# Kernel optimization log

Hardware: AMD Instinct MI355X
Metric: run time of the kernel (lower is better)

Reference implementation:

```python
import jax, jax.numpy as jnp
import numpy as np

EPS = 1e-06


def setup_inputs() -> dict:
    key = jax.random.key(0)
    k1, k2, k3 = jax.random.split(key, 3)
    B, V = 2048, 128
    pred_severity = jax.random.normal(k1, (B, V), dtype=jnp.float32)
    target_severity = jax.random.normal(k2, (B, V), dtype=jnp.float32)
    visit_mask = jax.random.randint(k3, (B, V), 0, 2).astype(jnp.int32)
    return {
        "pred_severity": pred_severity,
        "target_severity": target_severity,
        "visit_mask": visit_mask,
    }


def reference(pred_severity, target_severity, visit_mask):
    # pred_severity, target_severity: [B, V]; visit_mask: [B, V] (0/1)
    p, t = pred_severity, target_severity
    valid = visit_mask.astype(bool)
    V = p.shape[1]

    # Entry (b, i, j): delta_t = t[j] - t[i], dp = p[i] - p[j]
    dt = t[:, None, :] - t[:, :, None]          # [B, V, V]
    dp = p[:, :, None] - p[:, None, :]          # [B, V, V]
    sign = jnp.sign(dt)
    loss = jax.nn.softplus(-dp * sign)          # [B, V, V]

    tri = jnp.triu(jnp.ones((V, V), dtype=bool), k=1)  # ordered pairs i < j
    mask = (valid[:, :, None] & valid[:, None, :]
            & (jnp.abs(dt) > EPS) & tri)        # [B, V, V]

    total = jnp.sum(jnp.where(mask, loss, jnp.zeros((), loss.dtype)))
    count = jnp.sum(mask).astype(loss.dtype)
    return jnp.where(count > 0, total / count, jnp.zeros((), loss.dtype))
```

## Files before the change

kernel.cpp:

```cpp
#include <hip/hip_runtime.h>
#include <math.h>

#define PRL_EPS   1e-6f
#define PRL_B     2048
#define PRL_V     128
#define PRL_LOG2E 1.44269504088896340736f
#define PRL_LN2   0.69314718055994530942f

__global__ __launch_bounds__(256) void prl_pairs_kernel(
    const float* __restrict__ pred,
    const float* __restrict__ targ,
    const int*   __restrict__ mask,
    float*        __restrict__ psum,
    unsigned int* __restrict__ pcnt)
{
    __shared__ float2 rowdup[2][256];

    const int tid = threadIdx.x;
    const int r   = tid >> 7;
    const int x   = tid & 127;
    const int b   = blockIdx.x * 2 + r;

    const size_t base = (size_t)b * PRL_V + x;
    const float p  = pred[base];
    const float t  = targ[base];
    const int   m  = mask[base];
    const float tm = m ? t : __int_as_float(0x7fc00000);

    const float2 own = make_float2(p, tm);
    rowdup[r][x]       = own;
    rowdup[r][x + 128] = own;
    __syncthreads();

    const float2* __restrict__ rp = &rowdup[r][x];

    float        s[3] = {0.0f, 0.0f, 0.0f};
    unsigned int c[3] = {0u, 0u, 0u};

    for (int d0 = 1; d0 < 64; d0 += 9) {
        #pragma unroll
        for (int u = 0; u < 9; ++u) {
            const float2 e = rp[d0 + u];
            const float dt = e.y - tm;
            const float dp = p - e.x;
            const bool valid = fabsf(dt) > PRL_EPS;
            const float xx = (dt > 0.0f) ? -dp : dp;
            const float y  = xx * PRL_LOG2E;
            const float lg = __log2f(1.0f + exp2f(y));
            s[u % 3] += valid ? lg : 0.0f;
            c[u % 3] += valid ? 1u : 0u;
        }
    }
    if (x < 64) {
        const float2 e = rp[64];
        const float dt = e.y - tm;
        const float dp = p - e.x;
        const bool valid = fabsf(dt) > PRL_EPS;
        const float xx = (dt > 0.0f) ? -dp : dp;
        const float y  = xx * PRL_LOG2E;
        const float lg = __log2f(1.0f + exp2f(y));
        s[0] += valid ? lg : 0.0f;
        c[0] += valid ? 1u : 0u;
    }

    float        sum = (s[0] + s[1]) + s[2];
    unsigned int cnt = (c[0] + c[1]) + c[2];

    #pragma unroll
    for (int o = 32; o > 0; o >>= 1) {
        sum += __shfl_down(sum, o);
        cnt += __shfl_down(cnt, o);
    }

    __shared__ float        wsum[4];
    __shared__ unsigned int wcnt[4];
    const int wid  = tid >> 6;
    const int lane = tid & 63;
    if (lane == 0) { wsum[wid] = sum; wcnt[wid] = cnt; }
    __syncthreads();

    if (tid == 0) {
        psum[blockIdx.x] = (wsum[0] + wsum[1] + wsum[2] + wsum[3]) * PRL_LN2;
        pcnt[blockIdx.x] = wcnt[0] + wcnt[1] + wcnt[2] + wcnt[3];
    }
}

__global__ __launch_bounds__(256) void prl_reduce_kernel(
    const float*        __restrict__ psum,
    const unsigned int* __restrict__ pcnt,
    float* __restrict__ out)
{
    const int tid = threadIdx.x;

    const float4 v = ((const float4*)psum)[tid];
    const uint4  w = ((const uint4*)pcnt)[tid];
    float        ss = (v.x + v.y) + (v.z + v.w);
    unsigned int cc = (w.x + w.y) + (w.z + w.w);

    #pragma unroll
    for (int o = 32; o > 0; o >>= 1) {
        ss += __shfl_down(ss, o);
        cc += __shfl_down(cc, o);
    }

    __shared__ float        ws[4];
    __shared__ unsigned int wc[4];
    const int wid  = tid >> 6;
    const int lane = tid & 63;
    if (lane == 0) { ws[wid] = ss; wc[wid] = cc; }
    __syncthreads();

    if (tid == 0) {
        const float        S = ws[0] + ws[1] + ws[2] + ws[3];
        const unsigned int C = wc[0] + wc[1] + wc[2] + wc[3];
        out[0] = (C > 0) ? (S / (float)C) : 0.0f;
    }
}

extern "C" void kernel_launch(void* const* d_in, const int* in_sizes, int n_in,
                              void* d_out, int out_size, void* d_ws, size_t ws_size,
                              hipStream_t stream) {
    const float* pred = (const float*)d_in[0];
    const float* targ = (const float*)d_in[1];
    const int*   mask = (const int*)d_in[2];
    float* out = (float*)d_out;

    const int NBLK = PRL_B / 2;

    float*        psum = (float*)d_ws;
    unsigned int* pcnt = (unsigned int*)((char*)d_ws + NBLK * sizeof(float));

    prl_pairs_kernel<<<NBLK, 256, 0, stream>>>(pred, targ, mask, psum, pcnt);
    prl_reduce_kernel<<<1, 256, 0, stream>>>(psum, pcnt, out);
}
```

Baseline: 15.97 us.

## Fold softplus logs into products and split row-pair work across two blocks

Each thread now multiplies four (1+exp2) terms and takes one log2 per group, where it used to take one log2 per pair. That cuts transcendental work roughly by 40%. Pred is prescaled by log2e and the sign flip is done with a bit xor. The grid doubles, so each block handles half of the 64 cyclic offsets per row pair, and the reduction kernel reads 2048 partials. Clamping the exponent at 30 prevents overflow but changes precision for large margins.

```diff
diff --git a/kernel.cpp b/kernel.cpp
--- a/kernel.cpp
+++ b/kernel.cpp
@@ -6,6 +6,7 @@
 #define PRL_V     128
 #define PRL_LOG2E 1.44269504088896340736f
 #define PRL_LN2   0.69314718055994530942f
+#define PRL_NBLK  2048
 
 __global__ __launch_bounds__(256) void prl_pairs_kernel(
     const float* __restrict__ pred,
@@ -16,72 +17,71 @@
 {
     __shared__ float2 rowdup[2][256];
 
-    const int tid = threadIdx.x;
-    const int r   = tid >> 7;
-    const int x   = tid & 127;
-    const int b   = blockIdx.x * 2 + r;
+    const int tid  = threadIdx.x;
+    const int r    = tid >> 7;
+    const int x    = tid & 127;
+    const int bid  = blockIdx.x;
+    const int pair = bid >> 1;
+    const int h    = bid & 1;
+    const int b    = pair * 2 + r;
 
     const size_t base = (size_t)b * PRL_V + x;
-    const float p  = pred[base];
+    const float pj = pred[base] * PRL_LOG2E;
     const float t  = targ[base];
     const int   m  = mask[base];
     const float tm = m ? t : __int_as_float(0x7fc00000);
 
-    const float2 own = make_float2(p, tm);
+    const float2 own = make_float2(pj, tm);
     rowdup[r][x]       = own;
     rowdup[r][x + 128] = own;
     __syncthreads();
 
-    const float2* __restrict__ rp = &rowdup[r][x];
+    const float2* __restrict__ rp = &rowdup[r][x] + (1 + 32 * h);
+    const bool last_ok = (h == 0) | (x < 64);
 
-    float        s[3] = {0.0f, 0.0f, 0.0f};
-    unsigned int c[3] = {0u, 0u, 0u};
+    float        slog = 0.0f;
+    unsigned int cnt  = 0;
 
-    for (int d0 = 1; d0 < 64; d0 += 9) {
+    #pragma unroll
+    for (int g = 0; g < 8; ++g) {
+        float a[4];
         #pragma unroll
-        for (int u = 0; u < 9; ++u) {
-            const float2 e = rp[d0 + u];
-            const float dt = e.y - tm;
-            const float dp = p - e.x;
-            const bool valid = fabsf(dt) > PRL_EPS;
-            const float xx = (dt > 0.0f) ? -dp : dp;
-            const float y  = xx * PRL_LOG2E;
-            const float lg = __log2f(1.0f + exp2f(y));
-            s[u % 3] += valid ? lg : 0.0f;
-            c[u % 3] += valid ? 1u : 0u;
+        for (int u = 0; u < 4; ++u) {
+            const int dd = 4 * g + u;
+            const float2 e = rp[dd];
+            const float ndt = tm - e.y;
+            const float dpv = pj - e.x;
+            const unsigned sg = __float_as_uint(ndt) & 0x80000000u;
+            const float y = __uint_as_float(__float_as_uint(dpv) ^ sg);
+            bool valid = fabsf(ndt) > PRL_EPS;
+            if (g == 7 && u == 3) valid = valid && last_ok;
+            const float av = exp2f(fminf(y, 30.0f));
+            a[u] = valid ? av : 0.0f;
+            cnt += valid ? 1u : 0u;
         }
+        float q = 1.0f + a[0];
+        q = fmaf(q, a[1], q);
+        q = fmaf(q, a[2], q);
+        q = fmaf(q, a[3], q);
+        slog += __log2f(q);
     }
-    if (x < 64) {
-        const float2 e = rp[64];
-        const float dt = e.y - tm;
-        const float dp = p - e.x;
-        const bool valid = fabsf(dt) > PRL_EPS;
-        const float xx = (dt > 0.0f) ? -dp : dp;
-        const float y  = xx * PRL_LOG2E;
-        const float lg = __log2f(1.0f + exp2f(y));
-        s[0] += valid ? lg : 0.0f;
-        c[0] += valid ? 1u : 0u;
-    }
-
-    float        sum = (s[0] + s[1]) + s[2];
-    unsigned int cnt = (c[0] + c[1]) + c[2];
 
     #pragma unroll
     for (int o = 32; o > 0; o >>= 1) {
-        sum += __shfl_down(sum, o);
-        cnt += __shfl_down(cnt, o);
+        slog += __shfl_down(slog, o);
+        cnt  += __shfl_down(cnt, o);
     }
 
     __shared__ float        wsum[4];
     __shared__ unsigned int wcnt[4];
     const int wid  = tid >> 6;
     const int lane = tid & 63;
-    if (lane == 0) { wsum[wid] = sum; wcnt[wid] = cnt; }
+    if (lane == 0) { wsum[wid] = slog; wcnt[wid] = cnt; }
     __syncthreads();
 
     if (tid == 0) {
-        psum[blockIdx.x] = (wsum[0] + wsum[1] + wsum[2] + wsum[3]) * PRL_LN2;
-        pcnt[blockIdx.x] = wcnt[0] + wcnt[1] + wcnt[2] + wcnt[3];
+        psum[bid] = (wsum[0] + wsum[1] + wsum[2] + wsum[3]) * PRL_LN2;
+        pcnt[bid] = wcnt[0] + wcnt[1] + wcnt[2] + wcnt[3];
     }
 }
 
@@ -92,10 +92,15 @@
 {
     const int tid = threadIdx.x;
 
-    const float4 v = ((const float4*)psum)[tid];
-    const uint4  w = ((const uint4*)pcnt)[tid];
-    float        ss = (v.x + v.y) + (v.z + v.w);
-    unsigned int cc = (w.x + w.y) + (w.z + w.w);
+    float        ss = 0.0f;
+    unsigned int cc = 0;
+    #pragma unroll
+    for (int k = 0; k < PRL_NBLK / 1024; ++k) {
+        const float4 v = ((const float4*)psum)[tid + 256 * k];
+        const uint4  w = ((const uint4*)pcnt)[tid + 256 * k];
+        ss += (v.x + v.y) + (v.z + v.w);
+        cc += (w.x + w.y) + (w.z + w.w);
+    }
 
     #pragma unroll
     for (int o = 32; o > 0; o >>= 1) {
@@ -125,11 +130,9 @@
     const int*   mask = (const int*)d_in[2];
     float* out = (float*)d_out;
 
-    const int NBLK = PRL_B / 2;
+    float*        psum = (float*)d_ws;
+    unsigned int* pcnt = (unsigned int*)((char*)d_ws + PRL_NBLK * sizeof(float));
 
-    float*        psum = (float*)d_ws;
-    unsigned int* pcnt = (unsigned int*)((char*)d_ws + NBLK * sizeof(float));
-
-    prl_pairs_kernel<<<NBLK, 256, 0, stream>>>(pred, targ, mask, psum, pcnt);
+    prl_pairs_kernel<<<PRL_NBLK, 256, 0, stream>>>(pred, targ, mask, psum, pcnt);
     prl_reduce_kernel<<<1, 256, 0, stream>>>(psum, pcnt, out);
 }
```

Measured after the change: 15.17 us. -5.0%, faster.
